# Performance work log

Measured on AMD Instinct MI355X. Metric: run time of the kernel, lower is better.

Reference implementation:

```python
import jax, jax.numpy as jnp
import numpy as np

PAD = 16      # ReplicationPad2d(16)
KW = 33       # per-block kernel is 33x33
PATCH = 36    # 36x36 input patch per 4x4 output block
BLK = 4       # output block size


def setup_inputs() -> dict:
    key = jax.random.key(0)
    k1, k2 = jax.random.split(key)
    inputImg = jax.random.normal(k1, (1, 3, 512, 512), dtype=jnp.float32)
    Kernels = jax.random.uniform(k2, (1, KW * KW, 512 // BLK, 512 // BLK), dtype=jnp.float32)
    return {"inputImg": inputImg, "Kernels": Kernels}


def reference(inputImg, Kernels):
    B, C, H, W = inputImg.shape
    HB, WB = H // BLK, W // BLK
    # replication pad == edge pad
    padded = jnp.pad(inputImg, ((0, 0), (0, 0), (PAD, PAD), (PAD, PAD)), mode="edge")
    # gather overlapping 36x36 patches, one per 4x4 block (stride 4)
    idx_h = BLK * jnp.arange(HB)[:, None] + jnp.arange(PATCH)[None, :]  # [HB,36]
    idx_w = BLK * jnp.arange(WB)[:, None] + jnp.arange(PATCH)[None, :]  # [WB,36]
    tmp = padded[:, :, idx_h, :]            # [B,C,HB,36,Wp]
    patches = tmp[:, :, :, :, idx_w]        # [B,C,HB,36,WB,36]
    # per-block 33x33 kernel: Kernels[0, u*33+v, h, w] -> K[u,v,h,w]
    K = Kernels[0].reshape(KW, KW, HB, WB)
    # valid conv: out offset (oi,oj) in the 4x4 block
    rows = []
    for oi in range(BLK):
        cols = []
        for oj in range(BLK):
            win = patches[:, :, :, oi:oi + KW, :, oj:oj + KW]  # [B,C,HB,33,WB,33]
            cols.append(jnp.einsum("bchuwv,uvhw->bchw", win, K))
        rows.append(jnp.stack(cols, axis=-1))   # [B,C,HB,WB,4]
    out = jnp.stack(rows, axis=-2)              # [B,C,HB,WB,4,4]
    out = out.transpose(0, 1, 2, 4, 3, 5).reshape(B, C, H, W)
    return out
```

## Files before the change

### kernel.cpp

```cpp
#include <hip/hip_runtime.h>

#define HH 512
#define WW 512
#define PADDIM 544
#define PADELEMS (3 * PADDIM * PADDIM)
#define NB 128
#define KSTR 16384

__global__ __launch_bounds__(256) void pad_kernel(const float* __restrict__ img,
                                                  float* __restrict__ pad) {
    int idx = blockIdx.x * 256 + threadIdx.x;
    if (idx >= PADELEMS) return;
    int c  = idx / (PADDIM * PADDIM);
    int r  = idx - c * (PADDIM * PADDIM);
    int py = r / PADDIM;
    int px = r - py * PADDIM;
    int iy = min(max(py - 16, 0), HH - 1);
    int ix = min(max(px - 16, 0), WW - 1);
    pad[idx] = img[(c * HH + iy) * WW + ix];
}

__device__ __forceinline__ void async4(const float* g, float* l) {
    __builtin_amdgcn_global_load_lds((const __attribute__((address_space(1))) void*)g,
                                     (__attribute__((address_space(3))) void*)l, 4, 0, 0);
}
__device__ __forceinline__ void async16(const float* g, float* l) {
    __builtin_amdgcn_global_load_lds((const __attribute__((address_space(1))) void*)g,
                                     (__attribute__((address_space(3))) void*)l, 16, 0, 0);
}

__global__ __launch_bounds__(256, 2) void reblur_lds(const float* __restrict__ pad,
                                                     const float* __restrict__ Kern,
                                                     float* __restrict__ out) {
    __shared__ float s_w[2][33][64];
    __shared__ float s_img[3][8][288];

    const int lane = threadIdx.x & 63;
    const int dy   = threadIdx.x >> 6;
    const int half = blockIdx.x >> 8;
    const int bb   = blockIdx.x & 255;
    const int h    = bb >> 1;
    const int wt   = bb & 1;
    const int wb   = wt * 64 + lane;
    const int y    = 4 * h + dy;
    const int u0   = half ? 17 : 0;
    const int u1   = half ? 33 : 17;

    const int kofs = h * NB + wt * 64 + lane;

    for (int v = dy; v < 33; v += 4)
        async4(Kern + (u0 * 33 + v) * KSTR + kofs, &s_w[u0 & 1][v][0]);
    {
        const int p0 = 4 * h + u0;
        for (int k = dy; k < 12; k += 4) {
            const int c = k >> 2;
            const int p = p0 + (k & 3);
            const float* gb = pad + (c * PADDIM + p) * PADDIM + 256 * wt;
            float* lb = &s_img[c][p & 7][0];
            async16(gb + 4 * lane, lb);
            if (lane < 8) async16(gb + 256 + 4 * lane, lb + 256);
        }
    }

    float acc[3][4];
#pragma unroll
    for (int c = 0; c < 3; ++c)
#pragma unroll
        for (int oj = 0; oj < 4; ++oj) acc[c][oj] = 0.f;

#pragma unroll 1
    for (int u = u0; u < u1; ++u) {
        asm volatile("s_waitcnt vmcnt(0)" ::: "memory");
        __builtin_amdgcn_s_barrier();
        asm volatile("" ::: "memory");

        if (u + 1 < u1) {
            const int ku = u + 1;
            for (int v = dy; v < 33; v += 4)
                async4(Kern + (ku * 33 + v) * KSTR + kofs, &s_w[ku & 1][v][0]);
            if (dy < 3) {
                const int c = dy;
                const int p = 4 * h + u + 4;
                const float* gb = pad + (c * PADDIM + p) * PADDIM + 256 * wt;
                float* lb = &s_img[c][p & 7][0];
                async16(gb + 4 * lane, lb);
                if (lane < 8) async16(gb + 256 + 4 * lane, lb + 256);
            }
        }

        float wv[33];
#pragma unroll
        for (int v = 0; v < 33; ++v) wv[v] = s_w[u & 1][v][lane];
        const int slot = (4 * h + u + dy) & 7;
#pragma unroll
        for (int c = 0; c < 3; ++c) {
            const float4* rp = (const float4*)&s_img[c][slot][4 * lane];
            float row[36];
#pragma unroll
            for (int j = 0; j < 9; ++j) {
                const float4 t = rp[j];
                row[4 * j + 0] = t.x;
                row[4 * j + 1] = t.y;
                row[4 * j + 2] = t.z;
                row[4 * j + 3] = t.w;
            }
#pragma unroll
            for (int v = 0; v < 33; ++v)
#pragma unroll
                for (int oj = 0; oj < 4; ++oj)
                    acc[c][oj] = fmaf(row[v + oj], wv[v], acc[c][oj]);
        }
    }

#pragma unroll
    for (int c = 0; c < 3; ++c) {
        float* op = out + (c * HH + y) * WW + 4 * wb;
#pragma unroll
        for (int oj = 0; oj < 4; ++oj) atomicAdd(op + oj, acc[c][oj]);
    }
}

__global__ __launch_bounds__(256) void reblur_naive(const float* __restrict__ img,
                                                    const float* __restrict__ Kern,
                                                    float* __restrict__ out) {
    const int lane = threadIdx.x & 63;
    const int dy   = threadIdx.x >> 6;
    const int c    = blockIdx.x >> 8;
    const int bb   = blockIdx.x & 255;
    const int h    = bb >> 1;
    const int wt   = bb & 1;
    const int wb   = wt * 64 + lane;
    const int y    = 4 * h + dy;

    float acc[4] = {0.f, 0.f, 0.f, 0.f};
    const float* kb = Kern + h * NB + wb;
#pragma unroll 1
    for (int u = 0; u < 33; ++u) {
        const int iy = min(max(y + u - 16, 0), HH - 1);
        float row[36];
#pragma unroll
        for (int e = 0; e < 36; ++e) {
            const int ix = min(max(4 * wb + e - 16, 0), WW - 1);
            row[e]       = img[(c * HH + iy) * WW + ix];
        }
#pragma unroll
        for (int v = 0; v < 33; ++v) {
            const float w = kb[(u * 33 + v) * KSTR];
#pragma unroll
            for (int oj = 0; oj < 4; ++oj)
                acc[oj] = fmaf(row[v + oj], w, acc[oj]);
        }
    }
    float4 o;
    o.x = acc[0]; o.y = acc[1]; o.z = acc[2]; o.w = acc[3];
    *reinterpret_cast<float4*>(out + (c * HH + y) * WW + 4 * wb) = o;
}

extern "C" void kernel_launch(void* const* d_in, const int* in_sizes, int n_in,
                              void* d_out, int out_size, void* d_ws, size_t ws_size,
                              hipStream_t stream) {
    const float* img  = (const float*)d_in[0];
    const float* Kern = (const float*)d_in[1];
    float* out        = (float*)d_out;

    if (ws_size >= (size_t)PADELEMS * sizeof(float)) {
        float* pad = (float*)d_ws;
        hipMemsetAsync(d_out, 0, (size_t)out_size * sizeof(float), stream);
        pad_kernel<<<(PADELEMS + 255) / 256, 256, 0, stream>>>(img, pad);
        reblur_lds<<<512, 256, 0, stream>>>(pad, Kern, out);
    } else {
        reblur_naive<<<768, 256, 0, stream>>>(img, Kern, out);
    }
}
```

Measured before the change: 150.1 us.

## Store padded image as bf16 and restructure reblur into single-wave row-sliding blocks

The pad kernel now writes the padded image in bf16 with round-to-nearest-even and also zeroes the output, which removes the separate memset. The main kernel becomes 64-thread single-wave blocks that split the 36 padded rows into three slices of 12. Each block slides over padded rows and accumulates all four output rows per thread, reusing each image row across up to four kernel rows. It uses a 4-slot kernel-weight ring in LDS and no barriers. Converting the image to bf16 loses precision relative to the fp32 reference, and atomics now combine three partial sums per output.

```diff
diff --git a/kernel.cpp b/kernel.cpp
--- a/kernel.cpp
+++ b/kernel.cpp
@@ -2,122 +2,150 @@
 
 #define HH 512
 #define WW 512
-#define PADDIM 544
-#define PADELEMS (3 * PADDIM * PADDIM)
+#define PD 544
+#define PADN (3 * PD * PD)
+#define OUTN (3 * HH * WW)
 #define NB 128
 #define KSTR 16384
 
 __global__ __launch_bounds__(256) void pad_kernel(const float* __restrict__ img,
-                                                  float* __restrict__ pad) {
+                                                  unsigned short* __restrict__ gpad,
+                                                  float* __restrict__ out) {
     int idx = blockIdx.x * 256 + threadIdx.x;
-    if (idx >= PADELEMS) return;
-    int c  = idx / (PADDIM * PADDIM);
-    int r  = idx - c * (PADDIM * PADDIM);
-    int py = r / PADDIM;
-    int px = r - py * PADDIM;
+    if (idx < OUTN) out[idx] = 0.0f;
+    if (idx >= PADN) return;
+    int c  = idx / (PD * PD);
+    int r  = idx - c * (PD * PD);
+    int py = r / PD;
+    int px = r - py * PD;
     int iy = min(max(py - 16, 0), HH - 1);
     int ix = min(max(px - 16, 0), WW - 1);
-    pad[idx] = img[(c * HH + iy) * WW + ix];
+    union { float f; unsigned u; } v;
+    v.f = img[(c * HH + iy) * WW + ix];
+    unsigned u = v.u + 0x7FFFu + ((v.u >> 16) & 1u);
+    gpad[idx] = (unsigned short)(u >> 16);
 }
 
 __device__ __forceinline__ void async4(const float* g, float* l) {
     __builtin_amdgcn_global_load_lds((const __attribute__((address_space(1))) void*)g,
                                      (__attribute__((address_space(3))) void*)l, 4, 0, 0);
 }
-__device__ __forceinline__ void async16(const float* g, float* l) {
+__device__ __forceinline__ void async16u(const unsigned short* g, unsigned short* l) {
     __builtin_amdgcn_global_load_lds((const __attribute__((address_space(1))) void*)g,
                                      (__attribute__((address_space(3))) void*)l, 16, 0, 0);
 }
 
-__global__ __launch_bounds__(256, 2) void reblur_lds(const float* __restrict__ pad,
-                                                     const float* __restrict__ Kern,
-                                                     float* __restrict__ out) {
-    __shared__ float s_w[2][33][64];
-    __shared__ float s_img[3][8][288];
-
-    const int lane = threadIdx.x & 63;
-    const int dy   = threadIdx.x >> 6;
-    const int half = blockIdx.x >> 8;
+__device__ __forceinline__ float bflo(unsigned d) {
+    union { unsigned u; float f; } x; x.u = d << 16; return x.f;
+}
+__device__ __forceinline__ float bfhi(unsigned d) {
+    union { unsigned u; float f; } x; x.u = d & 0xFFFF0000u; return x.f;
+}
+
+__global__ __launch_bounds__(64) void reblur_kernel(const unsigned short* __restrict__ gpad,
+                                                    const float* __restrict__ Kern,
+                                                    float* __restrict__ out) {
+    __shared__ float s_w[4][33][64];
+    __shared__ unsigned short s_img[2][3][296];
+
+    const int lane = threadIdx.x;
+    const int s    = blockIdx.x >> 8;
     const int bb   = blockIdx.x & 255;
     const int h    = bb >> 1;
     const int wt   = bb & 1;
-    const int wb   = wt * 64 + lane;
-    const int y    = 4 * h + dy;
-    const int u0   = half ? 17 : 0;
-    const int u1   = half ? 33 : 17;
-
+    const int p0   = 12 * s;
+    const int p1   = p0 + 12;
     const int kofs = h * NB + wt * 64 + lane;
 
-    for (int v = dy; v < 33; v += 4)
-        async4(Kern + (u0 * 33 + v) * KSTR + kofs, &s_w[u0 & 1][v][0]);
-    {
-        const int p0 = 4 * h + u0;
-        for (int k = dy; k < 12; k += 4) {
-            const int c = k >> 2;
-            const int p = p0 + (k & 3);
-            const float* gb = pad + (c * PADDIM + p) * PADDIM + 256 * wt;
-            float* lb = &s_img[c][p & 7][0];
-            async16(gb + 4 * lane, lb);
-            if (lane < 8) async16(gb + 256 + 4 * lane, lb + 256);
+    for (int u = max(0, p0 - 3); u <= p0; ++u)
+        for (int v = 0; v < 33; ++v)
+            async4(Kern + ((u * 33 + v) * KSTR + kofs), &s_w[u & 3][v][0]);
+    if (lane < 36)
+        for (int c = 0; c < 3; ++c)
+            async16u(gpad + ((size_t)(c * PD + 4 * h + p0) * PD + 256 * wt) + 8 * lane,
+                     &s_img[p0 & 1][c][0]);
+
+    float acc[3][4][4];
+#pragma unroll
+    for (int c = 0; c < 3; ++c)
+#pragma unroll
+        for (int dy = 0; dy < 4; ++dy)
+#pragma unroll
+            for (int oj = 0; oj < 4; ++oj) acc[c][dy][oj] = 0.0f;
+
+#pragma unroll 1
+    for (int pp = p0; pp < p1; ++pp) {
+        asm volatile("s_waitcnt vmcnt(0)" ::: "memory");
+
+        float wreg[33];
+        const int u3 = pp - 3;
+        if (u3 >= 0) {
+#pragma unroll
+            for (int v = 0; v < 33; ++v) wreg[v] = s_w[u3 & 3][v][lane];
+        }
+        asm volatile("s_waitcnt lgkmcnt(0)" ::: "memory");
+
+        if (pp + 1 < p1) {
+            const int un = pp + 1;
+            if (un <= 32)
+                for (int v = 0; v < 33; ++v)
+                    async4(Kern + ((un * 33 + v) * KSTR + kofs), &s_w[un & 3][v][0]);
+            if (lane < 36)
+                for (int c = 0; c < 3; ++c)
+                    async16u(gpad + ((size_t)(c * PD + 4 * h + un) * PD + 256 * wt) + 8 * lane,
+                             &s_img[un & 1][c][0]);
+        }
+
+        float wf[3][36];
+        const int slot = pp & 1;
+#pragma unroll
+        for (int c = 0; c < 3; ++c) {
+#pragma unroll
+            for (int j = 0; j < 9; ++j) {
+                const uint2 d = *(const uint2*)&s_img[slot][c][4 * lane + 4 * j];
+                wf[c][4 * j + 0] = bflo(d.x);
+                wf[c][4 * j + 1] = bfhi(d.x);
+                wf[c][4 * j + 2] = bflo(d.y);
+                wf[c][4 * j + 3] = bfhi(d.y);
+            }
+        }
+
+#pragma unroll
+        for (int dy = 0; dy < 3; ++dy) {
+            const int u = pp - dy;
+            if (u >= 0 && u <= 32) {
+                const float* wp = &s_w[u & 3][0][lane];
+#pragma unroll
+                for (int v = 0; v < 33; ++v) {
+                    const float w = wp[v * 64];
+#pragma unroll
+                    for (int c = 0; c < 3; ++c)
+#pragma unroll
+                        for (int oj = 0; oj < 4; ++oj)
+                            acc[c][dy][oj] = fmaf(wf[c][v + oj], w, acc[c][dy][oj]);
+                }
+            }
+        }
+        if (u3 >= 0) {
+#pragma unroll
+            for (int v = 0; v < 33; ++v) {
+#pragma unroll
+                for (int c = 0; c < 3; ++c)
+#pragma unroll
+                    for (int oj = 0; oj < 4; ++oj)
+                        acc[c][3][oj] = fmaf(wf[c][v + oj], wreg[v], acc[c][3][oj]);
+            }
         }
     }
 
-    float acc[3][4];
 #pragma unroll
     for (int c = 0; c < 3; ++c)
 #pragma unroll
-        for (int oj = 0; oj < 4; ++oj) acc[c][oj] = 0.f;
-
-#pragma unroll 1
-    for (int u = u0; u < u1; ++u) {
-        asm volatile("s_waitcnt vmcnt(0)" ::: "memory");
-        __builtin_amdgcn_s_barrier();
-        asm volatile("" ::: "memory");
-
-        if (u + 1 < u1) {
-            const int ku = u + 1;
-            for (int v = dy; v < 33; v += 4)
-                async4(Kern + (ku * 33 + v) * KSTR + kofs, &s_w[ku & 1][v][0]);
-            if (dy < 3) {
-                const int c = dy;
-                const int p = 4 * h + u + 4;
-                const float* gb = pad + (c * PADDIM + p) * PADDIM + 256 * wt;
-                float* lb = &s_img[c][p & 7][0];
-                async16(gb + 4 * lane, lb);
-                if (lane < 8) async16(gb + 256 + 4 * lane, lb + 256);
-            }
-        }
-
-        float wv[33];
-#pragma unroll
-        for (int v = 0; v < 33; ++v) wv[v] = s_w[u & 1][v][lane];
-        const int slot = (4 * h + u + dy) & 7;
-#pragma unroll
-        for (int c = 0; c < 3; ++c) {
-            const float4* rp = (const float4*)&s_img[c][slot][4 * lane];
-            float row[36];
-#pragma unroll
-            for (int j = 0; j < 9; ++j) {
-                const float4 t = rp[j];
-                row[4 * j + 0] = t.x;
-                row[4 * j + 1] = t.y;
-                row[4 * j + 2] = t.z;
-                row[4 * j + 3] = t.w;
-            }
-#pragma unroll
-            for (int v = 0; v < 33; ++v)
-#pragma unroll
-                for (int oj = 0; oj < 4; ++oj)
-                    acc[c][oj] = fmaf(row[v + oj], wv[v], acc[c][oj]);
-        }
-    }
-
-#pragma unroll
-    for (int c = 0; c < 3; ++c) {
-        float* op = out + (c * HH + y) * WW + 4 * wb;
-#pragma unroll
-        for (int oj = 0; oj < 4; ++oj) atomicAdd(op + oj, acc[c][oj]);
-    }
+        for (int dy = 0; dy < 4; ++dy) {
+            float* op = out + (size_t)(c * HH + 4 * h + dy) * WW + 4 * (wt * 64 + lane);
+#pragma unroll
+            for (int oj = 0; oj < 4; ++oj) atomicAdd(op + oj, acc[c][dy][oj]);
+        }
 }
 
 __global__ __launch_bounds__(256) void reblur_naive(const float* __restrict__ img,
@@ -153,7 +181,7 @@
     }
     float4 o;
     o.x = acc[0]; o.y = acc[1]; o.z = acc[2]; o.w = acc[3];
-    *reinterpret_cast<float4*>(out + (c * HH + y) * WW + 4 * wb) = o;
+    *reinterpret_cast<float4*>(out + (size_t)(c * HH + y) * WW + 4 * wb) = o;
 }
 
 extern "C" void kernel_launch(void* const* d_in, const int* in_sizes, int n_in,
@@ -163,11 +191,10 @@
     const float* Kern = (const float*)d_in[1];
     float* out        = (float*)d_out;
 
-    if (ws_size >= (size_t)PADELEMS * sizeof(float)) {
-        float* pad = (float*)d_ws;
-        hipMemsetAsync(d_out, 0, (size_t)out_size * sizeof(float), stream);
-        pad_kernel<<<(PADELEMS + 255) / 256, 256, 0, stream>>>(img, pad);
-        reblur_lds<<<512, 256, 0, stream>>>(pad, Kern, out);
+    if (ws_size >= (size_t)PADN * sizeof(unsigned short)) {
+        unsigned short* gpad = (unsigned short*)d_ws;
+        pad_kernel<<<(PADN + 255) / 256, 256, 0, stream>>>(img, gpad, out);
+        reblur_kernel<<<768, 64, 0, stream>>>(gpad, Kern, out);
     } else {
         reblur_naive<<<768, 256, 0, stream>>>(img, Kern, out);
     }
```

Measured after the change: 160.1 us. +6.7%, slower.
